# Kernel tuning notes

Hardware: AMD Instinct MI355X
Metric: run time of the kernel (lower is better)

The kernel has to match this reference:

```python
import jax, jax.numpy as jnp
import numpy as np

B, G, I, E = 256, 24, 512, 512


def setup_inputs() -> dict:
    key = jax.random.key(0)
    k1, k2 = jax.random.split(key)
    inp = jax.random.normal(k1, (B, G, I), dtype=jnp.float32)
    weights = jax.random.normal(k2, (G, I, E), dtype=jnp.float32) * (1.0 / np.sqrt(E))
    bias = 0.1 * jnp.ones((E,), dtype=jnp.float32)
    # Cyclic group inverse-index table: row h is the permutation g -> (g - h) mod G,
    # matching symmetry_group.index2inverse_indices[h] (each row a valid permutation).
    g_ar = np.arange(G)
    inv_indices = jnp.asarray((g_ar[None, :] - g_ar[:, None]) % G, dtype=jnp.int32)
    return {"input": inp, "weights": weights, "bias": bias, "inv_indices": inv_indices}


def reference(input, weights, bias, inv_indices):
    # conv_filter[h, g, i, e] = weights[inv_indices[h, g], i, e]   -> [G, G, I, E]
    conv_filter = weights[inv_indices]
    # (input[:,None,:,:,None] * filter[None]).sum(2).sum(2) == einsum over g, i
    out = jnp.einsum("bgi,hgie->bhe", input, conv_filter)  # [B, G, E]
    return out + bias
```

## Files before the change

### kernel.cpp

```cpp
#include <hip/hip_runtime.h>
#include <hip/hip_bf16.h>
#include <stdint.h>

#define G_ 24
#define B_ 256
#define I_ 512
#define E_ 512
#define K_ (G_ * I_)
#define SPLITK 4
#define NTILES 48

typedef __hip_bfloat16 bf16;
typedef __bf16 bf16x8 __attribute__((ext_vector_type(8)));
typedef float f32x4 __attribute__((ext_vector_type(4)));

__global__ void cvt_in_kernel(const float* __restrict__ in, bf16* __restrict__ out, int n4) {
  int idx = blockIdx.x * blockDim.x + threadIdx.x;
  if (idx >= n4) return;
  float4 v = reinterpret_cast<const float4*>(in)[idx];
  union { bf16 h[4]; uint2 u; } pk;
  pk.h[0] = __float2bfloat16(v.x);
  pk.h[1] = __float2bfloat16(v.y);
  pk.h[2] = __float2bfloat16(v.z);
  pk.h[3] = __float2bfloat16(v.w);
  reinterpret_cast<uint2*>(out)[idx] = pk.u;
}

__global__ void transpose_w_kernel(const float* __restrict__ W, bf16* __restrict__ Wt) {
  __shared__ float tile[32][33];
  const int g = blockIdx.z;
  const int i0 = blockIdx.x * 32;
  const int e0 = blockIdx.y * 32;
  const float* src = W + (size_t)g * (I_ * E_) + (size_t)(i0 + threadIdx.y) * E_ + e0 + threadIdx.x;
  #pragma unroll
  for (int r = 0; r < 32; r += 8)
    tile[threadIdx.y + r][threadIdx.x] = src[(size_t)r * E_];
  __syncthreads();
  bf16* dst = Wt + (size_t)g * (I_ * E_) + (size_t)(e0 + threadIdx.y) * I_ + i0 + threadIdx.x;
  #pragma unroll
  for (int r = 0; r < 32; r += 8)
    dst[(size_t)r * I_] = __float2bfloat16(tile[threadIdx.x][threadIdx.y + r]);
}

__global__ void init_out_kernel(const float* __restrict__ bias, float* __restrict__ out, int n4) {
  int idx = blockIdx.x * blockDim.x + threadIdx.x;
  if (idx >= n4) return;
  int e4 = idx & 127;
  reinterpret_cast<float4*>(out)[idx] = reinterpret_cast<const float4*>(bias)[e4];
}

__global__ __launch_bounds__(256, 2) void gemm_kernel(
    const bf16* __restrict__ A,
    const bf16* __restrict__ Wt,
    float* __restrict__ out) {

  __shared__ __align__(16) bf16 lds[2][2][128 * 64];

  const int tid  = threadIdx.x;
  const int lane = tid & 63;
  const int wave = tid >> 6;
  const int wr   = wave >> 1;
  const int wc   = wave & 1;
  const int rsel = lane & 15;
  const int q    = lane >> 4;

  const int bid = blockIdx.x;
  const int swz = (bid & 7) * 96 + (bid >> 3);
  const int n0 = (swz & 3) * 128;
  const int m0 = ((swz >> 2) & 1) * 128;
  const int hs = swz >> 3;
  const int h  = hs >> 2;
  const int T0 = (hs & 3) * NTILES;

  f32x4 acc[4][4];
  #pragma unroll
  for (int i = 0; i < 4; ++i)
    #pragma unroll
    for (int j = 0; j < 4; ++j)
      acc[i][j] = (f32x4){0.f, 0.f, 0.f, 0.f};

  auto stage = [&](int t, int buf) {
    const int g  = t >> 3;
    const int i0 = (t & 7) * 64;
    int gsrc = g - h; if (gsrc < 0) gsrc += G_;
    const bf16* Abase = A  + (size_t)m0 * K_ + (size_t)t * 64;
    const bf16* Bbase = Wt + (size_t)gsrc * (I_ * E_) + (size_t)n0 * I_ + i0;
    #pragma unroll
    for (int j = 0; j < 4; ++j) {
      int c    = j * 256 + tid;
      int row  = c >> 3;
      int slot = (c & 7) ^ (row & 7);
      __builtin_amdgcn_global_load_lds(
          (const __attribute__((address_space(1))) void*)(Abase + (size_t)row * K_ + slot * 8),
          (__attribute__((address_space(3))) void*)&lds[buf][0][(size_t)c * 8], 16, 0, 0);
    }
    #pragma unroll
    for (int j = 0; j < 4; ++j) {
      int c    = j * 256 + tid;
      int row  = c >> 3;
      int slot = (c & 7) ^ (row & 7);
      __builtin_amdgcn_global_load_lds(
          (const __attribute__((address_space(1))) void*)(Bbase + (size_t)row * I_ + slot * 8),
          (__attribute__((address_space(3))) void*)&lds[buf][1][(size_t)c * 8], 16, 0, 0);
    }
  };

  stage(T0, 0);

  for (int lt = 0; lt < NTILES; ++lt) {
    const int cur = lt & 1;
    if (lt + 1 < NTILES) {
      stage(T0 + lt + 1, cur ^ 1);
      asm volatile("s_waitcnt vmcnt(8)" ::: "memory");
    } else {
      asm volatile("s_waitcnt vmcnt(0)" ::: "memory");
    }
    __builtin_amdgcn_s_barrier();
    asm volatile("" ::: "memory");

    const bf16* Al = &lds[cur][0][0];
    const bf16* Bl = &lds[cur][1][0];
    #pragma unroll
    for (int kk = 0; kk < 2; ++kk) {
      const int kslot = kk * 4 + q;
      bf16x8 af[4], bfr[4];
      #pragma unroll
      for (int mi = 0; mi < 4; ++mi) {
        int r = wr * 64 + mi * 16 + rsel;
        af[mi] = *(const bf16x8*)(Al + (size_t)r * 64 + (kslot ^ (r & 7)) * 8);
      }
      #pragma unroll
      for (int ni = 0; ni < 4; ++ni) {
        int r = wc * 64 + ni * 16 + rsel;
        bfr[ni] = *(const bf16x8*)(Bl + (size_t)r * 64 + (kslot ^ (r & 7)) * 8);
      }
      #pragma unroll
      for (int mi = 0; mi < 4; ++mi)
        #pragma unroll
        for (int ni = 0; ni < 4; ++ni)
          acc[mi][ni] = __builtin_amdgcn_mfma_f32_16x16x32_bf16(af[mi], bfr[ni], acc[mi][ni], 0, 0, 0);
    }

    asm volatile("s_waitcnt lgkmcnt(0)" ::: "memory");
    __builtin_amdgcn_s_barrier();
    asm volatile("" ::: "memory");
  }

  #pragma unroll
  for (int mi = 0; mi < 4; ++mi) {
    #pragma unroll
    for (int ni = 0; ni < 4; ++ni) {
      int ecol  = n0 + wc * 64 + ni * 16 + (lane & 15);
      int brow0 = m0 + wr * 64 + mi * 16 + (lane >> 4) * 4;
      float* o = out + (size_t)brow0 * (G_ * E_) + (size_t)h * E_ + ecol;
      #pragma unroll
      for (int r = 0; r < 4; ++r)
        atomicAdd(o + (size_t)r * (G_ * E_), acc[mi][ni][r]);
    }
  }
}

extern "C" void kernel_launch(void* const* d_in, const int* in_sizes, int n_in,
                              void* d_out, int out_size, void* d_ws, size_t ws_size,
                              hipStream_t stream) {
  const float* in   = (const float*)d_in[0];
  const float* w    = (const float*)d_in[1];
  const float* bias = (const float*)d_in[2];
  float* out = (float*)d_out;

  bf16* A_bf = (bf16*)d_ws;
  bf16* Wt   = (bf16*)((char*)d_ws + (size_t)B_ * K_ * 2);

  const int n4in  = (B_ * K_) / 4;
  const int n4out = (B_ * G_ * E_) / 4;
  cvt_in_kernel<<<n4in / 256, 256, 0, stream>>>(in, A_bf, n4in);
  transpose_w_kernel<<<dim3(E_ / 32, I_ / 32, G_), dim3(32, 8), 0, stream>>>(w, Wt);
  init_out_kernel<<<n4out / 256, 256, 0, stream>>>(bias, out, n4out);
  gemm_kernel<<<768, 256, 0, stream>>>(A_bf, Wt, out);
}
```

Before: 124.8 us.

## Halve K-tile to 32 for three blocks per CU and remap block indices by XCD

The GEMM now stages 128x32 bf16 tiles instead of 128x64, which halves LDS use so launch bounds can ask for 3 blocks per CU. The loop runs 96 shorter steps, unrolled by two with precomputed swizzled LDS offsets, and uses a new swizzle pattern suited to the narrower tile. Blocks are remapped so that each XCD owns one M-half and one K-split slice, meant to improve L2 reuse of A and W. In exchange there are twice as many barriers per K-range, and each step does less MFMA work to hide load latency.

```diff
diff --git a/kernel.cpp b/kernel.cpp
--- a/kernel.cpp
+++ b/kernel.cpp
@@ -7,8 +7,6 @@
 #define I_ 512
 #define E_ 512
 #define K_ (G_ * I_)
-#define SPLITK 4
-#define NTILES 48
 
 typedef __hip_bfloat16 bf16;
 typedef __bf16 bf16x8 __attribute__((ext_vector_type(8)));
@@ -49,12 +47,22 @@
   reinterpret_cast<float4*>(out)[idx] = reinterpret_cast<const float4*>(bias)[e4];
 }
 
-__global__ __launch_bounds__(256, 2) void gemm_kernel(
+#define FENCE() asm volatile("" ::: "memory")
+#define BAR()   __builtin_amdgcn_s_barrier()
+#define VMW(N)  asm volatile("s_waitcnt vmcnt(" #N ")" ::: "memory")
+
+__device__ __forceinline__ void gload16(const bf16* g, bf16* l) {
+  __builtin_amdgcn_global_load_lds((const __attribute__((address_space(1))) void*)g,
+                                   (__attribute__((address_space(3))) void*)l, 16, 0, 0);
+}
+
+__global__ __launch_bounds__(256, 3) void gemm_kernel(
     const bf16* __restrict__ A,
     const bf16* __restrict__ Wt,
     float* __restrict__ out) {
 
-  __shared__ __align__(16) bf16 lds[2][2][128 * 64];
+  __shared__ __align__(16) bf16 ldsA[2][128 * 32];
+  __shared__ __align__(16) bf16 ldsB[2][128 * 32];
 
   const int tid  = threadIdx.x;
   const int lane = tid & 63;
@@ -64,13 +72,31 @@
   const int rsel = lane & 15;
   const int q    = lane >> 4;
 
-  const int bid = blockIdx.x;
-  const int swz = (bid & 7) * 96 + (bid >> 3);
-  const int n0 = (swz & 3) * 128;
-  const int m0 = ((swz >> 2) & 1) * 128;
-  const int hs = swz >> 3;
-  const int h  = hs >> 2;
-  const int T0 = (hs & 3) * NTILES;
+  const int bid   = blockIdx.x;
+  const int xcd   = bid & 7;
+  const int m0    = (xcd & 1) * 128;
+  const int s     = xcd >> 1;
+  const int inner = bid >> 3;
+  const int n0    = (inner & 3) * 128;
+  const int h     = inner >> 2;
+
+  const int c0 = tid, c1 = tid + 256;
+  const size_t aoff0 = (size_t)(c0 >> 2) * K_ + (((c0 & 3) ^ ((c0 >> 3) & 3)) << 3);
+  const size_t aoff1 = (size_t)(c1 >> 2) * K_ + (((c1 & 3) ^ ((c1 >> 3) & 3)) << 3);
+  const size_t boff0 = (size_t)(c0 >> 2) * I_ + (((c0 & 3) ^ ((c0 >> 3) & 3)) << 3);
+  const size_t boff1 = (size_t)(c1 >> 2) * I_ + (((c1 & 3) ^ ((c1 >> 3) & 3)) << 3);
+
+  int aro[4], bro[4];
+  #pragma unroll
+  for (int mi = 0; mi < 4; ++mi) {
+    int r = wr * 64 + mi * 16 + rsel;
+    aro[mi] = r * 64 + ((q ^ ((r >> 1) & 3)) << 4);
+  }
+  #pragma unroll
+  for (int ni = 0; ni < 4; ++ni) {
+    int r = wc * 64 + ni * 16 + rsel;
+    bro[ni] = r * 64 + ((q ^ ((r >> 1) & 3)) << 4);
+  }
 
   f32x4 acc[4][4];
   #pragma unroll
@@ -79,79 +105,49 @@
     for (int j = 0; j < 4; ++j)
       acc[i][j] = (f32x4){0.f, 0.f, 0.f, 0.f};
 
-  auto stage = [&](int t, int buf) {
-    const int g  = t >> 3;
-    const int i0 = (t & 7) * 64;
-    int gsrc = g - h; if (gsrc < 0) gsrc += G_;
-    const bf16* Abase = A  + (size_t)m0 * K_ + (size_t)t * 64;
-    const bf16* Bbase = Wt + (size_t)gsrc * (I_ * E_) + (size_t)n0 * I_ + i0;
-    #pragma unroll
-    for (int j = 0; j < 4; ++j) {
-      int c    = j * 256 + tid;
-      int row  = c >> 3;
-      int slot = (c & 7) ^ (row & 7);
-      __builtin_amdgcn_global_load_lds(
-          (const __attribute__((address_space(1))) void*)(Abase + (size_t)row * K_ + slot * 8),
-          (__attribute__((address_space(3))) void*)&lds[buf][0][(size_t)c * 8], 16, 0, 0);
-    }
-    #pragma unroll
-    for (int j = 0; j < 4; ++j) {
-      int c    = j * 256 + tid;
-      int row  = c >> 3;
-      int slot = (c & 7) ^ (row & 7);
-      __builtin_amdgcn_global_load_lds(
-          (const __attribute__((address_space(1))) void*)(Bbase + (size_t)row * I_ + slot * 8),
-          (__attribute__((address_space(3))) void*)&lds[buf][1][(size_t)c * 8], 16, 0, 0);
-    }
+  auto stage = [&](int t, int b) {
+    const int gloc  = t >> 4;
+    const int gamma = t & 15;
+    int gsrc = s * 6 + gloc - h;
+    if (gsrc < 0) gsrc += G_;
+    if (gsrc >= G_) gsrc -= G_;
+    const bf16* Ab = A + (size_t)m0 * K_ + ((size_t)s * 96 + t) * 32;
+    const bf16* Bb = Wt + (size_t)gsrc * (I_ * E_) + (size_t)n0 * I_ + gamma * 32;
+    gload16(Ab + aoff0, &ldsA[b][(size_t)c0 * 8]);
+    gload16(Ab + aoff1, &ldsA[b][(size_t)c1 * 8]);
+    gload16(Bb + boff0, &ldsB[b][(size_t)c0 * 8]);
+    gload16(Bb + boff1, &ldsB[b][(size_t)c1 * 8]);
   };
 
-  stage(T0, 0);
+#define STEP(LT, CB, NB) do {                                                    \
+    if ((LT) + 1 < 96) { stage((LT) + 1, NB); VMW(4); } else { VMW(0); }         \
+    FENCE(); BAR(); FENCE();                                                     \
+    bf16x8 af[4], bfr[4];                                                        \
+    _Pragma("unroll") for (int mi = 0; mi < 4; ++mi)                             \
+      af[mi] = *(const bf16x8*)((const char*)(&ldsA[CB][0]) + aro[mi]);          \
+    _Pragma("unroll") for (int ni = 0; ni < 4; ++ni)                             \
+      bfr[ni] = *(const bf16x8*)((const char*)(&ldsB[CB][0]) + bro[ni]);         \
+    _Pragma("unroll") for (int mi = 0; mi < 4; ++mi)                             \
+      _Pragma("unroll") for (int ni = 0; ni < 4; ++ni)                           \
+        acc[mi][ni] = __builtin_amdgcn_mfma_f32_16x16x32_bf16(                   \
+            af[mi], bfr[ni], acc[mi][ni], 0, 0, 0);                              \
+    asm volatile("s_waitcnt lgkmcnt(0)" ::: "memory");                           \
+    BAR(); FENCE();                                                              \
+  } while (0)
 
-  for (int lt = 0; lt < NTILES; ++lt) {
-    const int cur = lt & 1;
-    if (lt + 1 < NTILES) {
-      stage(T0 + lt + 1, cur ^ 1);
-      asm volatile("s_waitcnt vmcnt(8)" ::: "memory");
-    } else {
-      asm volatile("s_waitcnt vmcnt(0)" ::: "memory");
-    }
-    __builtin_amdgcn_s_barrier();
-    asm volatile("" ::: "memory");
-
-    const bf16* Al = &lds[cur][0][0];
-    const bf16* Bl = &lds[cur][1][0];
-    #pragma unroll
-    for (int kk = 0; kk < 2; ++kk) {
-      const int kslot = kk * 4 + q;
-      bf16x8 af[4], bfr[4];
-      #pragma unroll
-      for (int mi = 0; mi < 4; ++mi) {
-        int r = wr * 64 + mi * 16 + rsel;
-        af[mi] = *(const bf16x8*)(Al + (size_t)r * 64 + (kslot ^ (r & 7)) * 8);
-      }
-      #pragma unroll
-      for (int ni = 0; ni < 4; ++ni) {
-        int r = wc * 64 + ni * 16 + rsel;
-        bfr[ni] = *(const bf16x8*)(Bl + (size_t)r * 64 + (kslot ^ (r & 7)) * 8);
-      }
-      #pragma unroll
-      for (int mi = 0; mi < 4; ++mi)
-        #pragma unroll
-        for (int ni = 0; ni < 4; ++ni)
-          acc[mi][ni] = __builtin_amdgcn_mfma_f32_16x16x32_bf16(af[mi], bfr[ni], acc[mi][ni], 0, 0, 0);
-    }
-
-    asm volatile("s_waitcnt lgkmcnt(0)" ::: "memory");
-    __builtin_amdgcn_s_barrier();
-    asm volatile("" ::: "memory");
+  stage(0, 0);
+  for (int lt = 0; lt < 96; lt += 2) {
+    STEP(lt, 0, 1);
+    STEP(lt + 1, 1, 0);
   }
+#undef STEP
 
   #pragma unroll
   for (int mi = 0; mi < 4; ++mi) {
     #pragma unroll
     for (int ni = 0; ni < 4; ++ni) {
-      int ecol  = n0 + wc * 64 + ni * 16 + (lane & 15);
-      int brow0 = m0 + wr * 64 + mi * 16 + (lane >> 4) * 4;
+      int ecol  = n0 + wc * 64 + ni * 16 + rsel;
+      int brow0 = m0 + wr * 64 + mi * 16 + q * 4;
       float* o = out + (size_t)brow0 * (G_ * E_) + (size_t)h * E_ + ecol;
       #pragma unroll
       for (int r = 0; r < 4; ++r)
```

After: 142.2 us. 1.14x slower.

## Enlarge GEMM tile to 256x256 with 512-thread blocks and precomputed LDS offsets

Applied to the files above, without the earlier changes.

Changes the block tile from 128x128 to 256x256 (full batch in M, half of E in N), using 8 waves each computing a 128x64 sub-tile, so 192 blocks are launched instead of 768. The larger tile doubles arithmetic intensity per LDS load and removes the M split. Global and LDS address offsets are also precomputed once outside the K loop. The trade-offs are 128 KB of LDS per block and more accumulator registers per thread, which lower occupancy, and only 192 blocks to fill the device.

```diff
diff --git a/kernel.cpp b/kernel.cpp
--- a/kernel.cpp
+++ b/kernel.cpp
@@ -7,8 +7,6 @@
 #define I_ 512
 #define E_ 512
 #define K_ (G_ * I_)
-#define SPLITK 4
-#define NTILES 48
 
 typedef __hip_bfloat16 bf16;
 typedef __bf16 bf16x8 __attribute__((ext_vector_type(8)));
@@ -49,109 +47,124 @@
   reinterpret_cast<float4*>(out)[idx] = reinterpret_cast<const float4*>(bias)[e4];
 }
 
-__global__ __launch_bounds__(256, 2) void gemm_kernel(
+#define FENCE() asm volatile("" ::: "memory")
+#define BAR()   __builtin_amdgcn_s_barrier()
+#define VMW(N)  asm volatile("s_waitcnt vmcnt(" #N ")" ::: "memory")
+
+__device__ __forceinline__ void gload16(const bf16* g, bf16* l) {
+  __builtin_amdgcn_global_load_lds((const __attribute__((address_space(1))) void*)g,
+                                   (__attribute__((address_space(3))) void*)l, 16, 0, 0);
+}
+
+__global__ __launch_bounds__(512, 2) void gemm256_kernel(
     const bf16* __restrict__ A,
     const bf16* __restrict__ Wt,
     float* __restrict__ out) {
 
-  __shared__ __align__(16) bf16 lds[2][2][128 * 64];
+  __shared__ __align__(16) bf16 lds[2][2][256 * 64];
 
   const int tid  = threadIdx.x;
   const int lane = tid & 63;
   const int wave = tid >> 6;
-  const int wr   = wave >> 1;
-  const int wc   = wave & 1;
+  const int wr   = wave >> 2;
+  const int wc   = wave & 3;
   const int rsel = lane & 15;
   const int q    = lane >> 4;
 
-  const int bid = blockIdx.x;
-  const int swz = (bid & 7) * 96 + (bid >> 3);
-  const int n0 = (swz & 3) * 128;
-  const int m0 = ((swz >> 2) & 1) * 128;
-  const int hs = swz >> 3;
-  const int h  = hs >> 2;
-  const int T0 = (hs & 3) * NTILES;
+  const int bid   = blockIdx.x;
+  const int xcd   = bid & 7;
+  const int n0    = (xcd & 1) * 256;
+  const int s     = xcd >> 1;
+  const int h     = bid >> 3;
+  const int T0    = s * 48;
 
-  f32x4 acc[4][4];
+  size_t aoff[4], boff[4];
+  int ldso[4];
   #pragma unroll
-  for (int i = 0; i < 4; ++i)
+  for (int j = 0; j < 4; ++j) {
+    int c    = tid + j * 512;
+    int row  = c >> 3;
+    int slot = (c & 7) ^ (row & 7);
+    aoff[j] = (size_t)row * K_ + slot * 8;
+    boff[j] = (size_t)row * I_ + slot * 8;
+    ldso[j] = c * 8;
+  }
+
+  int aro[8], bro[4];
+  #pragma unroll
+  for (int mi = 0; mi < 8; ++mi) {
+    int r = wr * 128 + mi * 16 + rsel;
+    aro[mi] = r * 128 + ((q ^ (r & 7)) << 4);
+  }
+  #pragma unroll
+  for (int ni = 0; ni < 4; ++ni) {
+    int r = wc * 64 + ni * 16 + rsel;
+    bro[ni] = r * 128 + ((q ^ (r & 7)) << 4);
+  }
+
+  f32x4 acc[8][4];
+  #pragma unroll
+  for (int i = 0; i < 8; ++i)
     #pragma unroll
     for (int j = 0; j < 4; ++j)
       acc[i][j] = (f32x4){0.f, 0.f, 0.f, 0.f};
 
-  auto stage = [&](int t, int buf) {
-    const int g  = t >> 3;
+  auto stage = [&](int t, int b) {
+    int g = t >> 3;
+    int gsrc = g - h; if (gsrc < 0) gsrc += G_;
     const int i0 = (t & 7) * 64;
-    int gsrc = g - h; if (gsrc < 0) gsrc += G_;
-    const bf16* Abase = A  + (size_t)m0 * K_ + (size_t)t * 64;
-    const bf16* Bbase = Wt + (size_t)gsrc * (I_ * E_) + (size_t)n0 * I_ + i0;
+    const bf16* Ab = A + (size_t)t * 64;
+    const bf16* Bb = Wt + (size_t)gsrc * (I_ * E_) + (size_t)n0 * I_ + i0;
     #pragma unroll
-    for (int j = 0; j < 4; ++j) {
-      int c    = j * 256 + tid;
-      int row  = c >> 3;
-      int slot = (c & 7) ^ (row & 7);
-      __builtin_amdgcn_global_load_lds(
-          (const __attribute__((address_space(1))) void*)(Abase + (size_t)row * K_ + slot * 8),
-          (__attribute__((address_space(3))) void*)&lds[buf][0][(size_t)c * 8], 16, 0, 0);
-    }
+    for (int j = 0; j < 4; ++j)
+      gload16(Ab + aoff[j], &lds[b][0][ldso[j]]);
     #pragma unroll
-    for (int j = 0; j < 4; ++j) {
-      int c    = j * 256 + tid;
-      int row  = c >> 3;
-      int slot = (c & 7) ^ (row & 7);
-      __builtin_amdgcn_global_load_lds(
-          (const __attribute__((address_space(1))) void*)(Bbase + (size_t)row * I_ + slot * 8),
-          (__attribute__((address_space(3))) void*)&lds[buf][1][(size_t)c * 8], 16, 0, 0);
-    }
+    for (int j = 0; j < 4; ++j)
+      gload16(Bb + boff[j], &lds[b][1][ldso[j]]);
   };
 
   stage(T0, 0);
 
-  for (int lt = 0; lt < NTILES; ++lt) {
+  for (int lt = 0; lt < 48; ++lt) {
     const int cur = lt & 1;
-    if (lt + 1 < NTILES) {
+    if (lt + 1 < 48) {
       stage(T0 + lt + 1, cur ^ 1);
-      asm volatile("s_waitcnt vmcnt(8)" ::: "memory");
+      VMW(8);
     } else {
-      asm volatile("s_waitcnt vmcnt(0)" ::: "memory");
+      VMW(0);
     }
-    __builtin_amdgcn_s_barrier();
-    asm volatile("" ::: "memory");
+    FENCE(); BAR(); FENCE();
 
-    const bf16* Al = &lds[cur][0][0];
-    const bf16* Bl = &lds[cur][1][0];
+    const char* Al = (const char*)&lds[cur][0][0];
+    const char* Bl = (const char*)&lds[cur][1][0];
     #pragma unroll
     for (int kk = 0; kk < 2; ++kk) {
-      const int kslot = kk * 4 + q;
-      bf16x8 af[4], bfr[4];
+      const int x = kk << 6;
+      bf16x8 af[8], bfr[4];
       #pragma unroll
-      for (int mi = 0; mi < 4; ++mi) {
-        int r = wr * 64 + mi * 16 + rsel;
-        af[mi] = *(const bf16x8*)(Al + (size_t)r * 64 + (kslot ^ (r & 7)) * 8);
-      }
+      for (int mi = 0; mi < 8; ++mi)
+        af[mi] = *(const bf16x8*)(Al + (aro[mi] ^ x));
       #pragma unroll
-      for (int ni = 0; ni < 4; ++ni) {
-        int r = wc * 64 + ni * 16 + rsel;
-        bfr[ni] = *(const bf16x8*)(Bl + (size_t)r * 64 + (kslot ^ (r & 7)) * 8);
-      }
+      for (int ni = 0; ni < 4; ++ni)
+        bfr[ni] = *(const bf16x8*)(Bl + (bro[ni] ^ x));
       #pragma unroll
-      for (int mi = 0; mi < 4; ++mi)
+      for (int mi = 0; mi < 8; ++mi)
         #pragma unroll
         for (int ni = 0; ni < 4; ++ni)
-          acc[mi][ni] = __builtin_amdgcn_mfma_f32_16x16x32_bf16(af[mi], bfr[ni], acc[mi][ni], 0, 0, 0);
+          acc[mi][ni] = __builtin_amdgcn_mfma_f32_16x16x32_bf16(
+              af[mi], bfr[ni], acc[mi][ni], 0, 0, 0);
     }
 
     asm volatile("s_waitcnt lgkmcnt(0)" ::: "memory");
-    __builtin_amdgcn_s_barrier();
-    asm volatile("" ::: "memory");
+    BAR(); FENCE();
   }
 
   #pragma unroll
-  for (int mi = 0; mi < 4; ++mi) {
+  for (int mi = 0; mi < 8; ++mi) {
     #pragma unroll
     for (int ni = 0; ni < 4; ++ni) {
-      int ecol  = n0 + wc * 64 + ni * 16 + (lane & 15);
-      int brow0 = m0 + wr * 64 + mi * 16 + (lane >> 4) * 4;
+      int ecol  = n0 + wc * 64 + ni * 16 + rsel;
+      int brow0 = wr * 128 + mi * 16 + q * 4;
       float* o = out + (size_t)brow0 * (G_ * E_) + (size_t)h * E_ + ecol;
       #pragma unroll
       for (int r = 0; r < 4; ++r)
@@ -176,5 +189,5 @@
   cvt_in_kernel<<<n4in / 256, 256, 0, stream>>>(in, A_bf, n4in);
   transpose_w_kernel<<<dim3(E_ / 32, I_ / 32, G_), dim3(32, 8), 0, stream>>>(w, Wt);
   init_out_kernel<<<n4out / 256, 256, 0, stream>>>(bias, out, n4out);
-  gemm_kernel<<<768, 256, 0, stream>>>(A_bf, Wt, out);
+  gemm256_kernel<<<192, 512, 0, stream>>>(A_bf, Wt, out);
 }
```

New measurement: 137.1 us. 9.8% more time.
